# Kernel tuning notes

Hardware: AMD Instinct MI355X
Metric: run time of the kernel (lower is better)

Reference implementation:

```python
import jax, jax.numpy as jnp
import numpy as np

N_HEAD = 8
WINDOW = 22   # sliding window size from get_mask()
TRAIN = 29    # per-segment length cap from get_mask()


def _build_mask(T):
    # Banded (sliding-window causal) mask on one segment, tiled 3x3 over segments.
    t = T // 3
    m = np.triu(np.ones((TRAIN, TRAIN), dtype=bool), 1)
    for i in range(WINDOW, TRAIN):
        m[i, : i - WINDOW + 1] = True
    m = np.tile(m[:t, :t], (3, 3))  # [T, T], True = masked out
    return jnp.asarray(m)


def setup_inputs() -> dict:
    key = jax.random.key(0)
    ks = jax.random.split(key, 5)
    B, T, C = 512, 87, 512
    s = 0.02
    return {
        "x": jax.random.normal(ks[0], (B, T, C), dtype=jnp.float32),
        "Wq": jax.random.normal(ks[1], (C, C), dtype=jnp.float32) * s,
        "bq": jnp.zeros((C,), dtype=jnp.float32),
        "Wk": jax.random.normal(ks[2], (C, C), dtype=jnp.float32) * s,
        "bk": jnp.zeros((C,), dtype=jnp.float32),
        "Wv": jax.random.normal(ks[3], (C, C), dtype=jnp.float32) * s,
        "bv": jnp.zeros((C,), dtype=jnp.float32),
        "Wp": jax.random.normal(ks[4], (C, C), dtype=jnp.float32) * s,
        "bp": jnp.zeros((C,), dtype=jnp.float32),
    }


def reference(x, Wq, bq, Wk, bk, Wv, bv, Wp, bp):
    B, T, C = x.shape
    H = N_HEAD
    D = C // H
    # nn.Linear: y = x @ W.T + b
    def split_heads(y):
        return y.reshape(B, T, H, D).transpose(0, 2, 1, 3)  # [B,H,T,D]
    q = split_heads(x @ Wq.T + bq)
    k = split_heads(x @ Wk.T + bk)
    v = split_heads(x @ Wv.T + bv)
    att = jnp.einsum("bhqd,bhkd->bhqk", q, k) * (1.0 / jnp.sqrt(jnp.float32(D)))
    mask = _build_mask(T)  # [T,T] True = disallowed
    att = jnp.where(mask[None, None], -jnp.inf, att)
    att = jax.nn.softmax(att, axis=-1)
    # dropout layers are identity in eval mode
    y = jnp.einsum("bhqk,bhkd->bhqd", att, v)
    y = y.transpose(0, 2, 1, 3).reshape(B, T, C)
    return y @ Wp.T + bp
```

## Files before the change

### kernel.cpp

```cpp
#include <hip/hip_runtime.h>
#include <hip/hip_bf16.h>
#include <stdint.h>

#define B_   512
#define T_   87
#define C_   512
#define H_   8
#define D_   64
#define BT_  44544
#define BH_  4096

typedef __attribute__((ext_vector_type(4))) float f32x4;
typedef __attribute__((ext_vector_type(8))) __bf16 bf16x8;
typedef __attribute__((ext_vector_type(4))) unsigned short u16x4;

__device__ __forceinline__ int mod29(int x) {
  return x < 29 ? x : (x < 58 ? x - 29 : x - 58);
}


__global__ void convert_x_kernel(const float* __restrict__ x,
                                 __hip_bfloat16* __restrict__ xb, int n4) {
  int stride = gridDim.x * blockDim.x;
  for (int i = blockIdx.x * blockDim.x + threadIdx.x; i < n4; i += stride) {
    f32x4 v = ((const f32x4*)x)[i];
    u16x4 o;
    o.x = __builtin_bit_cast(unsigned short, __float2bfloat16(v.x));
    o.y = __builtin_bit_cast(unsigned short, __float2bfloat16(v.y));
    o.z = __builtin_bit_cast(unsigned short, __float2bfloat16(v.z));
    o.w = __builtin_bit_cast(unsigned short, __float2bfloat16(v.w));
    ((u16x4*)xb)[i] = o;
  }
}

__global__ void convert_w_kernel(const float* __restrict__ Wq, const float* __restrict__ Wk,
                                 const float* __restrict__ Wv, const float* __restrict__ Wp,
                                 const float* __restrict__ bq, const float* __restrict__ bk,
                                 const float* __restrict__ bv,
                                 __hip_bfloat16* __restrict__ wqkv,
                                 __hip_bfloat16* __restrict__ wp,
                                 float* __restrict__ biasc) {
  const int NW = 262144;
  const int total = 3 * NW + NW + 1536;
  int stride = gridDim.x * blockDim.x;
  for (int i = blockIdx.x * blockDim.x + threadIdx.x; i < total; i += stride) {
    if (i < 3 * NW) {
      float v = (i < NW) ? Wq[i] : (i < 2 * NW ? Wk[i - NW] : Wv[i - 2 * NW]);
      wqkv[i] = __float2bfloat16(v);
    } else if (i < 4 * NW) {
      wp[i - 3 * NW] = __float2bfloat16(Wp[i - 3 * NW]);
    } else {
      int j = i - 4 * NW;
      biasc[j] = (j < 512) ? bq[j] : (j < 1024 ? bk[j - 512] : bv[j - 1024]);
    }
  }
}


template<int FM, int FN>
__device__ __forceinline__ void compute_tile(const char* Ab, const char* Bb,
                                             int wbM, int wbN, int r16, int r4,
                                             f32x4 acc[FM][FN]) {
  const int cxor = (r16 & 7) << 4;
  bf16x8 bf[FN][2];
#pragma unroll
  for (int fn = 0; fn < FN; ++fn) {
    int row = wbN + fn * 16 + r16;
#pragma unroll
    for (int kk = 0; kk < 2; ++kk)
      bf[fn][kk] = *(const bf16x8*)(Bb + row * 128 + ((kk * 64 + r4 * 16) ^ cxor));
  }
#pragma unroll
  for (int fm = 0; fm < FM; ++fm) {
    int row = wbM + fm * 16 + r16;
    bf16x8 a0 = *(const bf16x8*)(Ab + row * 128 + ((r4 * 16) ^ cxor));
    bf16x8 a1 = *(const bf16x8*)(Ab + row * 128 + ((64 + r4 * 16) ^ cxor));
#pragma unroll
    for (int fn = 0; fn < FN; ++fn) {
      acc[fm][fn] = __builtin_amdgcn_mfma_f32_16x16x32_bf16(a0, bf[fn][0], acc[fm][fn], 0, 0, 0);
      acc[fm][fn] = __builtin_amdgcn_mfma_f32_16x16x32_bf16(a1, bf[fn][1], acc[fm][fn], 0, 0, 0);
    }
  }
}

template<int EPI>
__global__ __launch_bounds__(256) void gemmr_kernel(
    const __hip_bfloat16* __restrict__ A, const __hip_bfloat16* __restrict__ Bt,
    const float* __restrict__ bias, int ntn,
    void* __restrict__ o0, void* __restrict__ o1, void* __restrict__ o2) {
  __shared__ __align__(16) char smem[2][2][16384];

  int tid = threadIdx.x, lane = tid & 63, wave = tid >> 6;
  int r16 = lane & 15, r4 = lane >> 4;

  int nwg = gridDim.x;
  int wg = (blockIdx.x & 7) * (nwg >> 3) + (blockIdx.x >> 3);
  int tileM = (wg / ntn) * 128, tileN = (wg % ntn) * 128;

  int wr = wave >> 1, wc = wave & 1;
  int wbM = wr * 64, wbN = wc * 64;

  const int rbase = tid >> 3, c = tid & 7;
  const int cs = (c ^ (rbase & 7)) << 4;
  const char* Ag = (const char*)A + (size_t)(tileM + rbase) * 1024 + c * 16;
  const char* Bg = (const char*)Bt + (size_t)(tileN + rbase) * 1024 + c * 16;

  f32x4 acc[4][4] = {};
  bf16x8 sA[2][4], sB[2][4];

#pragma unroll
  for (int j = 0; j < 4; ++j) {
    sA[0][j] = *(const bf16x8*)(Ag + (size_t)j * 32768);
    sB[0][j] = *(const bf16x8*)(Bg + (size_t)j * 32768);
  }
#pragma unroll
  for (int j = 0; j < 4; ++j) {
    *(bf16x8*)(&smem[0][0][0] + (rbase + 32 * j) * 128 + cs) = sA[0][j];
    *(bf16x8*)(&smem[0][1][0] + (rbase + 32 * j) * 128 + cs) = sB[0][j];
  }
#pragma unroll
  for (int j = 0; j < 4; ++j) {
    sA[1][j] = *(const bf16x8*)(Ag + (size_t)j * 32768 + 128);
    sB[1][j] = *(const bf16x8*)(Bg + (size_t)j * 32768 + 128);
  }
  __syncthreads();

#pragma unroll
  for (int kt = 0; kt < 8; ++kt) {
    const int cur = kt & 1;
    if (kt < 6) {
#pragma unroll
      for (int j = 0; j < 4; ++j) {
        sA[cur][j] = *(const bf16x8*)(Ag + (size_t)j * 32768 + (kt + 2) * 128);
        sB[cur][j] = *(const bf16x8*)(Bg + (size_t)j * 32768 + (kt + 2) * 128);
      }
    }
    __builtin_amdgcn_s_setprio(1);
    compute_tile<4, 4>(&smem[cur][0][0], &smem[cur][1][0], wbM, wbN, r16, r4, acc);
    __builtin_amdgcn_s_setprio(0);
    if (kt < 7) {
#pragma unroll
      for (int j = 0; j < 4; ++j) {
        *(bf16x8*)(&smem[cur ^ 1][0][0] + (rbase + 32 * j) * 128 + cs) = sA[cur ^ 1][j];
        *(bf16x8*)(&smem[cur ^ 1][1][0] + (rbase + 32 * j) * 128 + cs) = sB[cur ^ 1][j];
      }
    }
    __syncthreads();
  }

  if constexpr (EPI == 0) {
    char* scratch = &smem[0][0][0] + wave * 2304;
    int gn0 = tileN + wbN;
    int sel = gn0 >> 9;
    int hh = (gn0 & 511) >> 6;
    __hip_bfloat16* obase = (sel == 0) ? (__hip_bfloat16*)o0
                          : (sel == 1) ? (__hip_bfloat16*)o1 : (__hip_bfloat16*)o2;
#pragma unroll
    for (int fm = 0; fm < 4; ++fm) {
#pragma unroll
      for (int fn = 0; fn < 4; ++fn) {
        float bv = bias[gn0 + fn * 16 + r16];
#pragma unroll
        for (int rr = 0; rr < 4; ++rr)
          *(__hip_bfloat16*)(scratch + (r4 * 4 + rr) * 144 + (fn * 16 + r16) * 2) =
              __float2bfloat16(acc[fm][fn][rr] + bv);
      }
#pragma unroll
      for (int p = 0; p < 2; ++p) {
        bf16x8 vrow = *(const bf16x8*)(scratch + (p * 8 + (lane >> 3)) * 144 + (lane & 7) * 16);
        int gm = tileM + wbM + fm * 16 + p * 8 + (lane >> 3);
        int bb = gm / 87, tt = gm - bb * 87;
        *(bf16x8*)(obase + ((size_t)(bb * 8 + hh) * 96 + tt) * 64 + (lane & 7) * 8) = vrow;
      }
    }
  } else {
    char* scratch = &smem[0][0][0] + wave * 4352;
#pragma unroll
    for (int fm = 0; fm < 4; ++fm) {
#pragma unroll
      for (int fn = 0; fn < 4; ++fn) {
        float bv = bias[tileN + wbN + fn * 16 + r16];
#pragma unroll
        for (int rr = 0; rr < 4; ++rr)
          *(float*)(scratch + (r4 * 4 + rr) * 272 + (fn * 16 + r16) * 4) =
              acc[fm][fn][rr] + bv;
      }
#pragma unroll
      for (int p = 0; p < 4; ++p) {
        f32x4 vr = *(const f32x4*)(scratch + (p * 4 + (lane >> 4)) * 272 + (lane & 15) * 16);
        int gm = tileM + wbM + fm * 16 + p * 4 + (lane >> 4);
        *(f32x4*)((float*)o0 + (size_t)gm * 512 + tileN + wbN + (lane & 15) * 4) = vr;
      }
    }
  }
}

#define QS_O  0
#define KS_O  13824
#define VT_O  27648
#define PB_O  40960

__global__ __launch_bounds__(256) void attn_kernel(
    const __hip_bfloat16* __restrict__ q_ws, const __hip_bfloat16* __restrict__ k_ws,
    const __hip_bfloat16* __restrict__ v_ws, __hip_bfloat16* __restrict__ y_ws) {
  __shared__ __align__(16) char smem[60928];

  int tid = threadIdx.x, lane = tid & 63, wave = tid >> 6;
  int bh = blockIdx.x, b = bh >> 3, h = bh & 7;
  int r16 = lane & 15, r4 = lane >> 4;

  {
    const bf16x8* gq = (const bf16x8*)(q_ws + (size_t)bh * 6144);
    const bf16x8* gk = (const bf16x8*)(k_ws + (size_t)bh * 6144);
    const bf16x8* gv = (const bf16x8*)(v_ws + (size_t)bh * 6144);
    for (int i = tid; i < 768; i += 256) {
      int row = i >> 3, ch = i & 7;
      *(bf16x8*)(smem + QS_O + row * 144 + ch * 16) = gq[i];
      *(bf16x8*)(smem + KS_O + row * 144 + ch * 16) = gk[i];
      bf16x8 v8 = gv[i];
      int tc = row >> 3, tb = (row & 7) << 1, xr = ch & 3;
#pragma unroll
      for (int e = 0; e < 8; ++e) {
        int d = ch * 8 + e;
        *(__bf16*)(smem + VT_O + d * 208 + ((tc ^ xr) << 4) + tb) = v8[e];
      }
    }
  }
  __syncthreads();

  int ljv[6]; bool cok[6];
#pragma unroll
  for (int j = 0; j < 6; ++j) {
    int col = j * 16 + r16;
    ljv[j] = mod29(col);
    cok[j] = col < 87;
  }

  for (int m = wave; m < 6; m += 4) {
    f32x4 s[6] = {};
#pragma unroll
    for (int kk = 0; kk < 2; ++kk) {
      bf16x8 aq = *(const bf16x8*)(smem + QS_O + (m * 16 + r16) * 144 + kk * 64 + r4 * 16);
#pragma unroll
      for (int j = 0; j < 6; ++j) {
        bf16x8 kb = *(const bf16x8*)(smem + KS_O + (j * 16 + r16) * 144 + kk * 64 + r4 * 16);
        s[j] = __builtin_amdgcn_mfma_f32_16x16x32_bf16(aq, kb, s[j], 0, 0, 0);
      }
    }
#pragma unroll
    for (int rr = 0; rr < 4; ++rr) {
      int row = m * 16 + r4 * 4 + rr;
      bool rok = row < 87;
      int lr = mod29(row);
      float mxv = -1e30f;
#pragma unroll
      for (int j = 0; j < 6; ++j) {
        bool al = rok && cok[j] && (ljv[j] <= lr) && (ljv[j] + 21 >= lr);
        float sv = al ? s[j][rr] * 0.125f : -1e30f;
        s[j][rr] = sv;
        mxv = fmaxf(mxv, sv);
      }
      mxv = fmaxf(mxv, __shfl_xor(mxv, 1));
      mxv = fmaxf(mxv, __shfl_xor(mxv, 2));
      mxv = fmaxf(mxv, __shfl_xor(mxv, 4));
      mxv = fmaxf(mxv, __shfl_xor(mxv, 8));
      float sm = 0.f;
#pragma unroll
      for (int j = 0; j < 6; ++j) {
        float e = __expf(s[j][rr] - mxv);
        s[j][rr] = e;
        sm += e;
      }
      sm += __shfl_xor(sm, 1);
      sm += __shfl_xor(sm, 2);
      sm += __shfl_xor(sm, 4);
      sm += __shfl_xor(sm, 8);
      float inv = rok ? 1.f / sm : 0.f;
#pragma unroll
      for (int j = 0; j < 6; ++j)
        *(__hip_bfloat16*)(smem + PB_O + row * 208 + (j * 16 + r16) * 2) =
            __float2bfloat16(s[j][rr] * inv);
    }
  }
  __syncthreads();

  for (int p = 0; p < 6; ++p) {
    int pair = wave + p * 4;
    int mt = pair >> 2, nt = pair & 3;
    int d = nt * 16 + r16;
    int dx = (d >> 3) & 3;
    f32x4 acc = {0.f, 0.f, 0.f, 0.f};
#pragma unroll
    for (int kk = 0; kk < 3; ++kk) {
      bf16x8 a  = *(const bf16x8*)(smem + PB_O + (mt * 16 + r16) * 208 + kk * 64 + r4 * 16);
      bf16x8 bb = *(const bf16x8*)(smem + VT_O + d * 208 + (((kk * 4 + r4) ^ dx) << 4));
      acc = __builtin_amdgcn_mfma_f32_16x16x32_bf16(a, bb, acc, 0, 0, 0);
    }
    int t0 = mt * 16 + r4 * 4;
#pragma unroll
    for (int r = 0; r < 4; ++r)
      *(__bf16*)(smem + QS_O + (t0 + r) * 136 + d * 2) =
          __builtin_bit_cast(__bf16, __builtin_bit_cast(unsigned short, __float2bfloat16(acc[r])));
  }
  __syncthreads();

  for (int i = tid; i < 768; i += 256) {
    int row = i >> 3, ch = i & 7;
    if (row < 87) {
      bf16x8 vrow = *(const bf16x8*)(smem + QS_O + row * 136 + ch * 16);
      *(bf16x8*)((char*)y_ws + ((size_t)b * 87 + row) * 1024 + h * 128 + ch * 16) = vrow;
    }
  }
}

extern "C" void kernel_launch(void* const* d_in, const int* in_sizes, int n_in,
                              void* d_out, int out_size, void* d_ws, size_t ws_size,
                              hipStream_t stream) {
  const float* x  = (const float*)d_in[0];
  const float* Wq = (const float*)d_in[1];
  const float* bq = (const float*)d_in[2];
  const float* Wk = (const float*)d_in[3];
  const float* bk = (const float*)d_in[4];
  const float* Wv = (const float*)d_in[5];
  const float* bv = (const float*)d_in[6];
  const float* Wp = (const float*)d_in[7];
  const float* bp = (const float*)d_in[8];
  float* out = (float*)d_out;

  char* ws = (char*)d_ws;
  size_t off = 0;
  __hip_bfloat16* xb    = (__hip_bfloat16*)(ws + off); off += (size_t)BT_ * 512 * 2;
  __hip_bfloat16* wqkv  = (__hip_bfloat16*)(ws + off); off += 1536 * 512 * 2;
  __hip_bfloat16* wp    = (__hip_bfloat16*)(ws + off); off += 512 * 512 * 2;
  float*          biasc = (float*)(ws + off);          off += 8192;
  __hip_bfloat16* q_ws  = (__hip_bfloat16*)(ws + off); off += (size_t)BH_ * 6144 * 2;
  __hip_bfloat16* k_ws  = (__hip_bfloat16*)(ws + off); off += (size_t)BH_ * 6144 * 2;
  __hip_bfloat16* v_ws  = (__hip_bfloat16*)(ws + off); off += (size_t)BH_ * 6144 * 2;
  __hip_bfloat16* yb = xb;

  if (ws_size < off) return;

  convert_x_kernel<<<2048, 256, 0, stream>>>(x, xb, BT_ * 512 / 4);
  convert_w_kernel<<<1024, 256, 0, stream>>>(Wq, Wk, Wv, Wp, bq, bk, bv, wqkv, wp, biasc);
  gemmr_kernel<0><<<4176, 256, 0, stream>>>(xb, wqkv, biasc, 12, q_ws, k_ws, v_ws);
  attn_kernel<<<BH_, 256, 0, stream>>>(q_ws, k_ws, v_ws, yb);
  gemmr_kernel<1><<<1392, 256, 0, stream>>>(yb, wp, bp, 4, out, nullptr, nullptr);
}
```

Before: 240.3 us.

## Enlarge GEMM tiles to 256x128 with 32-wide K steps and single-stage register prefetch

The projection GEMMs now use 256x128 output tiles, with each wave computing 128x64 (8x4 MFMA fragments). The K dimension is walked in 16 steps of 32 instead of 8 steps of 64, and the LDS layout uses 64-byte rows with a new XOR swizzle. Global loads are prefetched only one step ahead, and grid sizes are halved to match. The aim is more reuse of each loaded tile and fewer workgroups, at the cost of more accumulator registers, lower occupancy and twice as many barriers per tile.

```diff
diff --git a/kernel.cpp b/kernel.cpp
--- a/kernel.cpp
+++ b/kernel.cpp
@@ -57,106 +57,103 @@
 }
 
 
-template<int FM, int FN>
-__device__ __forceinline__ void compute_tile(const char* Ab, const char* Bb,
-                                             int wbM, int wbN, int r16, int r4,
-                                             f32x4 acc[FM][FN]) {
-  const int cxor = (r16 & 7) << 4;
-  bf16x8 bf[FN][2];
-#pragma unroll
-  for (int fn = 0; fn < FN; ++fn) {
-    int row = wbN + fn * 16 + r16;
-#pragma unroll
-    for (int kk = 0; kk < 2; ++kk)
-      bf[fn][kk] = *(const bf16x8*)(Bb + row * 128 + ((kk * 64 + r4 * 16) ^ cxor));
-  }
-#pragma unroll
-  for (int fm = 0; fm < FM; ++fm) {
-    int row = wbM + fm * 16 + r16;
-    bf16x8 a0 = *(const bf16x8*)(Ab + row * 128 + ((r4 * 16) ^ cxor));
-    bf16x8 a1 = *(const bf16x8*)(Ab + row * 128 + ((64 + r4 * 16) ^ cxor));
-#pragma unroll
-    for (int fn = 0; fn < FN; ++fn) {
-      acc[fm][fn] = __builtin_amdgcn_mfma_f32_16x16x32_bf16(a0, bf[fn][0], acc[fm][fn], 0, 0, 0);
-      acc[fm][fn] = __builtin_amdgcn_mfma_f32_16x16x32_bf16(a1, bf[fn][1], acc[fm][fn], 0, 0, 0);
-    }
-  }
-}
-
 template<int EPI>
-__global__ __launch_bounds__(256) void gemmr_kernel(
+__global__ __launch_bounds__(256) void gemmk_kernel(
     const __hip_bfloat16* __restrict__ A, const __hip_bfloat16* __restrict__ Bt,
     const float* __restrict__ bias, int ntn,
     void* __restrict__ o0, void* __restrict__ o1, void* __restrict__ o2) {
-  __shared__ __align__(16) char smem[2][2][16384];
+  constexpr int BUFB = 24576;
+  constexpr int BOFF = 16384;
+  __shared__ __align__(16) char smem[2 * BUFB];
 
   int tid = threadIdx.x, lane = tid & 63, wave = tid >> 6;
   int r16 = lane & 15, r4 = lane >> 4;
 
   int nwg = gridDim.x;
   int wg = (blockIdx.x & 7) * (nwg >> 3) + (blockIdx.x >> 3);
-  int tileM = (wg / ntn) * 128, tileN = (wg % ntn) * 128;
+  int tileM = (wg / ntn) * 256, tileN = (wg % ntn) * 128;
 
   int wr = wave >> 1, wc = wave & 1;
-  int wbM = wr * 64, wbN = wc * 64;
-
-  const int rbase = tid >> 3, c = tid & 7;
-  const int cs = (c ^ (rbase & 7)) << 4;
-  const char* Ag = (const char*)A + (size_t)(tileM + rbase) * 1024 + c * 16;
-  const char* Bg = (const char*)Bt + (size_t)(tileN + rbase) * 1024 + c * 16;
-
-  f32x4 acc[4][4] = {};
-  bf16x8 sA[2][4], sB[2][4];
-
-#pragma unroll
-  for (int j = 0; j < 4; ++j) {
-    sA[0][j] = *(const bf16x8*)(Ag + (size_t)j * 32768);
-    sB[0][j] = *(const bf16x8*)(Bg + (size_t)j * 32768);
-  }
-#pragma unroll
-  for (int j = 0; j < 4; ++j) {
-    *(bf16x8*)(&smem[0][0][0] + (rbase + 32 * j) * 128 + cs) = sA[0][j];
-    *(bf16x8*)(&smem[0][1][0] + (rbase + 32 * j) * 128 + cs) = sB[0][j];
-  }
-#pragma unroll
-  for (int j = 0; j < 4; ++j) {
-    sA[1][j] = *(const bf16x8*)(Ag + (size_t)j * 32768 + 128);
-    sB[1][j] = *(const bf16x8*)(Bg + (size_t)j * 32768 + 128);
-  }
+  int wbM = wr * 128, wbN = wc * 64;
+
+  const int rb = tid >> 2, cc = tid & 3;
+  const int csA = ((cc ^ ((rb >> 1) & 3)) << 4);
+  const char* AgBase = (const char*)A + (size_t)(tileM + rb) * 1024 + cc * 16;
+  const char* BgBase = (const char*)Bt + (size_t)(tileN + rb) * 1024 + cc * 16;
+
+  f32x4 acc[8][4] = {};
+  bf16x8 sA[4], sB[2];
+
+  int arow[8], brow[4];
+#pragma unroll
+  for (int fm = 0; fm < 8; ++fm) arow[fm] = wbM + fm * 16 + r16;
+#pragma unroll
+  for (int fn = 0; fn < 4; ++fn) brow[fn] = wbN + fn * 16 + r16;
+
+#pragma unroll
+  for (int j = 0; j < 4; ++j) sA[j] = *(const bf16x8*)(AgBase + (size_t)j * 65536);
+#pragma unroll
+  for (int j = 0; j < 2; ++j) sB[j] = *(const bf16x8*)(BgBase + (size_t)j * 65536);
+#pragma unroll
+  for (int j = 0; j < 4; ++j)
+    *(bf16x8*)(smem + (rb + 64 * j) * 64 + csA) = sA[j];
+#pragma unroll
+  for (int j = 0; j < 2; ++j)
+    *(bf16x8*)(smem + BOFF + (rb + 64 * j) * 64 + csA) = sB[j];
   __syncthreads();
 
 #pragma unroll
-  for (int kt = 0; kt < 8; ++kt) {
+  for (int kt = 0; kt < 16; ++kt) {
     const int cur = kt & 1;
-    if (kt < 6) {
-#pragma unroll
-      for (int j = 0; j < 4; ++j) {
-        sA[cur][j] = *(const bf16x8*)(Ag + (size_t)j * 32768 + (kt + 2) * 128);
-        sB[cur][j] = *(const bf16x8*)(Bg + (size_t)j * 32768 + (kt + 2) * 128);
-      }
-    }
-    __builtin_amdgcn_s_setprio(1);
-    compute_tile<4, 4>(&smem[cur][0][0], &smem[cur][1][0], wbM, wbN, r16, r4, acc);
-    __builtin_amdgcn_s_setprio(0);
-    if (kt < 7) {
-#pragma unroll
-      for (int j = 0; j < 4; ++j) {
-        *(bf16x8*)(&smem[cur ^ 1][0][0] + (rbase + 32 * j) * 128 + cs) = sA[cur ^ 1][j];
-        *(bf16x8*)(&smem[cur ^ 1][1][0] + (rbase + 32 * j) * 128 + cs) = sB[cur ^ 1][j];
-      }
+    if (kt < 15) {
+#pragma unroll
+      for (int j = 0; j < 4; ++j)
+        sA[j] = *(const bf16x8*)(AgBase + (size_t)j * 65536 + (kt + 1) * 64);
+#pragma unroll
+      for (int j = 0; j < 2; ++j)
+        sB[j] = *(const bf16x8*)(BgBase + (size_t)j * 65536 + (kt + 1) * 64);
+    }
+    {
+      const char* Ab = smem + cur * BUFB;
+      const char* Bb = Ab + BOFF;
+      bf16x8 bfr[4];
+#pragma unroll
+      for (int fn = 0; fn < 4; ++fn)
+        bfr[fn] = *(const bf16x8*)(Bb + brow[fn] * 64 +
+                                   ((r4 ^ ((brow[fn] >> 1) & 3)) << 4));
+      __builtin_amdgcn_s_setprio(1);
+#pragma unroll
+      for (int fm = 0; fm < 8; ++fm) {
+        bf16x8 a = *(const bf16x8*)(Ab + arow[fm] * 64 +
+                                    ((r4 ^ ((arow[fm] >> 1) & 3)) << 4));
+#pragma unroll
+        for (int fn = 0; fn < 4; ++fn)
+          acc[fm][fn] = __builtin_amdgcn_mfma_f32_16x16x32_bf16(a, bfr[fn],
+                                                                acc[fm][fn], 0, 0, 0);
+      }
+      __builtin_amdgcn_s_setprio(0);
+    }
+    if (kt < 15) {
+      char* nb = smem + (cur ^ 1) * BUFB;
+#pragma unroll
+      for (int j = 0; j < 4; ++j)
+        *(bf16x8*)(nb + (rb + 64 * j) * 64 + csA) = sA[j];
+#pragma unroll
+      for (int j = 0; j < 2; ++j)
+        *(bf16x8*)(nb + BOFF + (rb + 64 * j) * 64 + csA) = sB[j];
     }
     __syncthreads();
   }
 
   if constexpr (EPI == 0) {
-    char* scratch = &smem[0][0][0] + wave * 2304;
+    char* scratch = smem + wave * 2304;
     int gn0 = tileN + wbN;
     int sel = gn0 >> 9;
     int hh = (gn0 & 511) >> 6;
     __hip_bfloat16* obase = (sel == 0) ? (__hip_bfloat16*)o0
                           : (sel == 1) ? (__hip_bfloat16*)o1 : (__hip_bfloat16*)o2;
 #pragma unroll
-    for (int fm = 0; fm < 4; ++fm) {
+    for (int fm = 0; fm < 8; ++fm) {
 #pragma unroll
       for (int fn = 0; fn < 4; ++fn) {
         float bv = bias[gn0 + fn * 16 + r16];
@@ -174,9 +171,9 @@
       }
     }
   } else {
-    char* scratch = &smem[0][0][0] + wave * 4352;
-#pragma unroll
-    for (int fm = 0; fm < 4; ++fm) {
+    char* scratch = smem + wave * 4352;
+#pragma unroll
+    for (int fm = 0; fm < 8; ++fm) {
 #pragma unroll
       for (int fn = 0; fn < 4; ++fn) {
         float bv = bias[tileN + wbN + fn * 16 + r16];
@@ -342,7 +339,7 @@
 
   convert_x_kernel<<<2048, 256, 0, stream>>>(x, xb, BT_ * 512 / 4);
   convert_w_kernel<<<1024, 256, 0, stream>>>(Wq, Wk, Wv, Wp, bq, bk, bv, wqkv, wp, biasc);
-  gemmr_kernel<0><<<4176, 256, 0, stream>>>(xb, wqkv, biasc, 12, q_ws, k_ws, v_ws);
+  gemmk_kernel<0><<<2088, 256, 0, stream>>>(xb, wqkv, biasc, 12, q_ws, k_ws, v_ws);
   attn_kernel<<<BH_, 256, 0, stream>>>(q_ws, k_ws, v_ws, yb);
-  gemmr_kernel<1><<<1392, 256, 0, stream>>>(yb, wp, bp, 4, out, nullptr, nullptr);
-}
+  gemmk_kernel<1><<<696, 256, 0, stream>>>(yb, wp, bp, 4, out, nullptr, nullptr);
+}
```

New measurement: 274.6 us. 1.14x slower.
